# Kernel tuning notes

Measured on AMD Instinct MI355X. Metric: run time of the kernel, lower is better.

Reference implementation:

```python
import jax, jax.numpy as jnp
import numpy as np

N = 256      # Lx * Ly sites
NH = 64      # GRU hidden units
K = 2        # local Hilbert space dim


def setup_inputs() -> dict:
    key = jax.random.key(0)
    k1, k2, k3, k4, k5 = jax.random.split(key, 5)
    # scale weights down to keep sigmoid/tanh/softmax in a sane range
    return {
        "numsamples": 8192,
        "Wi": jax.random.normal(k1, (K, 3 * NH), jnp.float32) * 0.1,
        "Wh": jax.random.normal(k2, (NH, 3 * NH), jnp.float32) * 0.1,
        "b": jax.random.normal(k3, (2, 3 * NH), jnp.float32) * 0.1,
        "Wd": jax.random.normal(k4, (NH, K), jnp.float32) * 0.1,
        "bd": jax.random.normal(k5, (K,), jnp.float32) * 0.1,
    }


def _gru_cell(x, h, Wi, Wh, b):
    # keras GRU with reset_after=True (default)
    mx = x @ Wi + b[0]           # [B, 3*NH]
    mh = h @ Wh + b[1]           # [B, 3*NH]
    xz, xr, xh = jnp.split(mx, 3, axis=-1)
    rz, rr, rh = jnp.split(mh, 3, axis=-1)
    z = jax.nn.sigmoid(xz + rz)
    r = jax.nn.sigmoid(xr + rr)
    hh = jnp.tanh(xh + r * rh)
    return z * h + (1.0 - z) * hh


def reference(numsamples, Wi, Wh, b, Wd, bd):
    B = numsamples
    keys = jax.random.split(jax.random.key(1234), N)

    def step(carry, key):
        h, inp = carry                         # h: [B,NH], inp: [B,K] one-hot
        h = _gru_cell(inp, h, Wi, Wh, b)
        logits = h @ Wd + bd                   # [B,K]
        logp = jax.nn.log_softmax(logits)      # log of dense-softmax output
        s = jax.random.categorical(key, logits)  # [B] int
        chosen = jnp.take_along_axis(logp, s[:, None], axis=1)[:, 0]
        inp_new = jax.nn.one_hot(s, K, dtype=jnp.float32)
        return (h, inp_new), (s, chosen)

    h0 = jnp.zeros((B, NH), jnp.float32)
    inp0 = jnp.zeros((B, K), jnp.float32)
    _, (samples, chosen_logp) = jax.lax.scan(step, (h0, inp0), keys)
    samples = samples.T.astype(jnp.float32)           # [B, N]
    log_probs = 0.5 * jnp.sum(chosen_logp, axis=0)    # [B]
    return samples, log_probs
```

## Files before the change

kernel.cpp:

```cpp
#include <hip/hip_runtime.h>
#include <stdint.h>

#define NSITES 256
#define NHID   64
#define BATCH  8192

typedef float v4f __attribute__((ext_vector_type(4)));
typedef short v8s __attribute__((ext_vector_type(8)));

__device__ __forceinline__ uint32_t rotl32(uint32_t v, int d) {
  return (v << d) | (v >> (32 - d));
}

__device__ __forceinline__ void tf2x32(uint32_t k0, uint32_t k1,
                                       uint32_t x0, uint32_t x1,
                                       uint32_t& o0, uint32_t& o1) {
  uint32_t ks2 = k0 ^ k1 ^ 0x1BD11BDAu;
  x0 += k0; x1 += k1;
#define TFR4(a,b,c,d) \
  x0 += x1; x1 = rotl32(x1,a); x1 ^= x0; \
  x0 += x1; x1 = rotl32(x1,b); x1 ^= x0; \
  x0 += x1; x1 = rotl32(x1,c); x1 ^= x0; \
  x0 += x1; x1 = rotl32(x1,d); x1 ^= x0;
  TFR4(13,15,26,6)   x0 += k1;  x1 += ks2 + 1u;
  TFR4(17,29,16,24)  x0 += ks2; x1 += k0  + 2u;
  TFR4(13,15,26,6)   x0 += k0;  x1 += k1  + 3u;
  TFR4(17,29,16,24)  x0 += k1;  x1 += ks2 + 4u;
  TFR4(13,15,26,6)   x0 += ks2; x1 += k0  + 5u;
#undef TFR4
  o0 = x0; o1 = x1;
}

__device__ __forceinline__ float gumb_from_bits(uint32_t bits) {
  float f = __uint_as_float((bits >> 9) | 0x3f800000u) - 1.0f;
  float u = (f == 0.0f) ? 1.17549435e-38f : f;
  return -logf(-logf(u));
}

__device__ __forceinline__ uint32_t rbits32(uint32_t k0, uint32_t k1, uint32_t e) {
  uint32_t a, b;
  tf2x32(k0, k1, 0u, e, a, b);
  return a ^ b;
}

__global__ void split_awt(const float* __restrict__ Wh, const float* __restrict__ Wd,
                          ushort* __restrict__ w0, ushort* __restrict__ w1,
                          ushort* __restrict__ w2) {
  int idx = blockIdx.x * 256 + threadIdx.x;
  if (idx >= 208 * 64) return;
  int col = idx >> 6;
  int j   = idx & 63;
  float w;
  if (col < 192) {
    w = Wh[j * 192 + col];
  } else {
    const int which = (col - 192) & 3;
    w = (which == 0) ? Wd[j * 2] : (which == 1) ? Wd[j * 2 + 1] : 0.0f;
  }
  uint32_t u0 = __float_as_uint(w) & 0xffff0000u;
  float f0 = __uint_as_float(u0);
  float r1 = w - f0;
  uint32_t u1 = __float_as_uint(r1) & 0xffff0000u;
  float f1 = __uint_as_float(u1);
  float r2 = r1 - f1;
  uint32_t u2 = __float_as_uint(r2) & 0xffff0000u;
  w0[idx] = (ushort)(u0 >> 16);
  w1[idx] = (ushort)(u1 >> 16);
  w2[idx] = (ushort)(u2 >> 16);
}

__device__ __forceinline__ float sigmoid_xla(float x) {
  return 0.5f + 0.5f * tanhf(0.5f * x);
}

#define MF(A_, B_, C_) __builtin_amdgcn_mfma_f32_16x16x32_bf16((A_), (B_), (C_), 0, 0, 0)
#define F4(v_, r_) (((const float*)&(v_))[r_])

__global__ __launch_bounds__(256, 2)
void rnn_mfma9(const float* __restrict__ Wi, const float* __restrict__ bb,
               const float* __restrict__ bd,
               const ushort* __restrict__ w0p, const ushort* __restrict__ w1p,
               const ushort* __restrict__ w2p,
               float* __restrict__ out_s, float* __restrict__ out_lp) {
  __shared__ __align__(16) ushort bsp[2][3072];
  __shared__ __align__(16) float2 gl[NSITES * 16];
  __shared__ __align__(16) float c0zr[128];
  __shared__ __align__(16) float bh0a[64], bh1a[64];
  __shared__ __align__(16) float cw0[192], cw1[192];

  const int tid = threadIdx.x;
  const int l = tid & 63, s = l & 15, hi = l >> 4;
  const int w = tid >> 6;
  const int base = blockIdx.x * 16;

  if (tid < 64) {
    c0zr[tid] = bb[tid] + bb[192 + tid];
    c0zr[tid + 64] = bb[tid + 64] + bb[256 + tid];
    bh0a[tid] = bb[128 + tid];
    bh1a[tid] = bb[320 + tid];
    cw0[tid] = Wi[tid]; cw0[tid + 64] = Wi[tid + 64]; cw0[tid + 128] = Wi[tid + 128];
    cw1[tid] = Wi[192 + tid]; cw1[tid + 64] = Wi[256 + tid]; cw1[tid + 128] = Wi[320 + tid];
  }
  for (int k = tid; k < 1536; k += 256) ((uint*)bsp[0])[k] = 0u;

  {
    uint32_t kt0, kt1;
    tf2x32(0u, 1234u, 0u, (uint32_t)tid, kt0, kt1);
    for (int k = 0; k < 16; ++k) {
      const int bidx = base + k;
      const float g0 = gumb_from_bits(rbits32(kt0, kt1, (uint32_t)(2 * bidx)));
      const float g1 = gumb_from_bits(rbits32(kt0, kt1, (uint32_t)(2 * bidx + 1)));
      gl[tid * 16 + k] = make_float2(g0, g1);
    }
  }
  __syncthreads();

  v8s A0[3][2], A1[3][2], A2[3][2];
#pragma unroll
  for (int i3 = 0; i3 < 3; ++i3) {
    const int tile = w + 4 * i3;
#pragma unroll
    for (int kc = 0; kc < 2; ++kc) {
      const int off = (16 * tile + s) * 64 + 32 * kc + 8 * hi;
      A0[i3][kc] = *reinterpret_cast<const v8s*>(w0p + off);
      A1[i3][kc] = *reinterpret_cast<const v8s*>(w1p + off);
      A2[i3][kc] = *reinterpret_cast<const v8s*>(w2p + off);
    }
  }
  v8s L0[2], L1[2], L2[2];
#pragma unroll
  for (int kc = 0; kc < 2; ++kc) {
    const int off = (192 + s) * 64 + 32 * kc + 8 * hi;
    L0[kc] = *reinterpret_cast<const v8s*>(w0p + off);
    L1[kc] = *reinterpret_cast<const v8s*>(w1p + off);
    L2[kc] = *reinterpret_cast<const v8s*>(w2p + off);
  }

  const float bd0 = bd[0], bd1 = bd[1];
  const int u0i = 16 * w + 4 * hi;
  const float4 czv  = *reinterpret_cast<const float4*>(&c0zr[u0i]);
  const float4 crv  = *reinterpret_cast<const float4*>(&c0zr[64 + u0i]);
  const float4 bh0v = *reinterpret_cast<const float4*>(&bh0a[u0i]);
  const float4 bh1v = *reinterpret_cast<const float4*>(&bh1a[u0i]);
  const float4 wz0  = *reinterpret_cast<const float4*>(&cw0[u0i]);
  const float4 wz1  = *reinterpret_cast<const float4*>(&cw1[u0i]);
  const float4 wr0  = *reinterpret_cast<const float4*>(&cw0[64 + u0i]);
  const float4 wr1  = *reinterpret_cast<const float4*>(&cw1[64 + u0i]);
  const float4 wh0  = *reinterpret_cast<const float4*>(&cw0[128 + u0i]);
  const float4 wh1  = *reinterpret_cast<const float4*>(&cw1[128 + u0i]);

  const int kcw = w >> 1;
  const int hgw = (2 * w + (hi >> 1)) & 3;
  const int i0  = (hi & 1) * 4;

  float hreg[4] = {0.0f, 0.0f, 0.0f, 0.0f};
  float lp = 0.0f;
  int p = 0;

  for (int t = 0; t <= NSITES; ++t) {
    const ushort* rb = bsp[p] + hi * 128 + s * 8;
    v8s B0[2], B1[2], B2[2];
#pragma unroll
    for (int kc = 0; kc < 2; ++kc) {
      B0[kc] = *reinterpret_cast<const v8s*>(rb + kc * 512);
      B1[kc] = *reinterpret_cast<const v8s*>(rb + 1024 + kc * 512);
      B2[kc] = *reinterpret_cast<const v8s*>(rb + 2048 + kc * 512);
    }

    v4f al = {0.0f, 0.0f, 0.0f, 0.0f};
#pragma unroll
    for (int kc = 0; kc < 2; ++kc) al = MF(L1[kc], B1[kc], al);
#pragma unroll
    for (int kc = 0; kc < 2; ++kc) al = MF(L2[kc], B0[kc], al);
#pragma unroll
    for (int kc = 0; kc < 2; ++kc) al = MF(L0[kc], B2[kc], al);
#pragma unroll
    for (int kc = 0; kc < 2; ++kc) al = MF(L1[kc], B0[kc], al);
#pragma unroll
    for (int kc = 0; kc < 2; ++kc) al = MF(L0[kc], B1[kc], al);
#pragma unroll
    for (int kc = 0; kc < 2; ++kc) al = MF(L0[kc], B0[kc], al);

    v4f acc[3];
    if (t < NSITES) {
#pragma unroll
      for (int i3 = 0; i3 < 3; ++i3) {
        v4f a = {0.0f, 0.0f, 0.0f, 0.0f};
#pragma unroll
        for (int kc = 0; kc < 2; ++kc) a = MF(A2[i3][kc], B0[kc], a);
#pragma unroll
        for (int kc = 0; kc < 2; ++kc) a = MF(A0[i3][kc], B2[kc], a);
#pragma unroll
        for (int kc = 0; kc < 2; ++kc) a = MF(A1[i3][kc], B1[kc], a);
#pragma unroll
        for (int kc = 0; kc < 2; ++kc) a = MF(A1[i3][kc], B0[kc], a);
#pragma unroll
        for (int kc = 0; kc < 2; ++kc) a = MF(A0[i3][kc], B1[kc], a);
#pragma unroll
        for (int kc = 0; kc < 2; ++kc) a = MF(A0[i3][kc], B0[kc], a);
        acc[i3] = a;
      }
    }

    int scd = 0;
    if (t > 0) {
      const float2 gc = gl[(t - 1) * 16 + s];
      const float l0 = al[0] + bd0, l1 = al[1] + bd1;
      const float mmax = fmaxf(l0, l1);
      const float sh0 = l0 - mmax, sh1 = l1 - mmax;
      const float lse = logf(expf(sh0) + expf(sh1));
      scd = ((l1 + gc.y) > (l0 + gc.x)) ? 1 : 0;
      lp += (scd ? sh1 : sh0) - lse;
      if (tid < 16) out_s[(size_t)(base + s) * NSITES + (t - 1)] = (float)scd;
    }

    if (t < NSITES) {
      float selz[4], selr[4], selh[4];
      if (t == 0) {
#pragma unroll
        for (int r = 0; r < 4; ++r) { selz[r] = 0.0f; selr[r] = 0.0f; selh[r] = 0.0f; }
      } else {
#pragma unroll
        for (int r = 0; r < 4; ++r) {
          selz[r] = scd ? F4(wz1, r) : F4(wz0, r);
          selr[r] = scd ? F4(wr1, r) : F4(wr0, r);
          selh[r] = scd ? F4(wh1, r) : F4(wh0, r);
        }
      }

      uint sp0[4], sp1[4], sp2[4];
#pragma unroll
      for (int r = 0; r < 4; ++r) {
        const float zin = acc[0][r] + F4(czv, r) + selz[r];
        const float rin = acc[1][r] + F4(crv, r) + selr[r];
        const float rhv = acc[2][r] + F4(bh1v, r);
        const float xhv = F4(bh0v, r) + selh[r];
        const float zg = sigmoid_xla(zin);
        const float rg = sigmoid_xla(rin);
        const float hg = tanhf(xhv + rg * rhv);
        const float hn = zg * hreg[r] + (1.0f - zg) * hg;
        hreg[r] = hn;
        const uint u0 = __float_as_uint(hn) & 0xffff0000u;
        const float f0 = __uint_as_float(u0);
        const float r1f = hn - f0;
        const uint u1 = __float_as_uint(r1f) & 0xffff0000u;
        const float f1 = __uint_as_float(u1);
        const float r2f = r1f - f1;
        const uint u2 = __float_as_uint(r2f) & 0xffff0000u;
        sp0[r] = u0 >> 16; sp1[r] = u1 >> 16; sp2[r] = u2 >> 16;
      }
      ushort* wb = bsp[p ^ 1] + kcw * 512 + hgw * 128 + s * 8 + i0;
      {
        uint2 q;
        q.x = sp0[0] | (sp0[1] << 16); q.y = sp0[2] | (sp0[3] << 16);
        *reinterpret_cast<uint2*>(wb) = q;
        q.x = sp1[0] | (sp1[1] << 16); q.y = sp1[2] | (sp1[3] << 16);
        *reinterpret_cast<uint2*>(wb + 1024) = q;
        q.x = sp2[0] | (sp2[1] << 16); q.y = sp2[2] | (sp2[3] << 16);
        *reinterpret_cast<uint2*>(wb + 2048) = q;
      }
    }

    __syncthreads();
    p ^= 1;
  }

  if (tid < 16) out_lp[base + s] = 0.5f * lp;
}

__global__ __launch_bounds__(64)
void rnn_plain(const float* __restrict__ Wi, const float* __restrict__ Wh,
               const float* __restrict__ bb, const float* __restrict__ Wd,
               const float* __restrict__ bd,
               float* __restrict__ out_s, float* __restrict__ out_lp) {
  const int lane = threadIdx.x;
  const int b = blockIdx.x;

  float wz[NHID], wr[NHID], wh[NHID];
#pragma unroll
  for (int j = 0; j < NHID; ++j) {
    wz[j] = Wh[j * 192 + lane];
    wr[j] = Wh[j * 192 + 64 + lane];
    wh[j] = Wh[j * 192 + 128 + lane];
  }
  const float b1z = bb[192 + lane];
  const float b1r = bb[192 + 64 + lane];
  const float b1h = bb[192 + 128 + lane];
  const float m0z = bb[lane], m0r = bb[64 + lane], m0h = bb[128 + lane];
  const float m1z = Wi[lane] + m0z, m1r = Wi[64 + lane] + m0r, m1h = Wi[128 + lane] + m0h;
  const float m2z = Wi[192 + lane] + m0z, m2r = Wi[192 + 64 + lane] + m0r,
              m2h = Wi[192 + 128 + lane] + m0h;
  const float wd0 = Wd[lane * 2 + 0], wd1 = Wd[lane * 2 + 1];
  const float bd0 = bd[0], bd1 = bd[1];

  float h = 0.0f, lpsum = 0.0f;
  float xz = m0z, xr = m0r, xh = m0h;

  for (int t = 0; t < NSITES; ++t) {
    uint32_t kt0, kt1;
    tf2x32(0u, 1234u, 0u, (uint32_t)t, kt0, kt1);
    const float g0 = gumb_from_bits(rbits32(kt0, kt1, (uint32_t)(2 * b)));
    const float g1 = gumb_from_bits(rbits32(kt0, kt1, (uint32_t)(2 * b + 1)));

    float az = 0.0f, ar = 0.0f, ah = 0.0f;
#pragma unroll
    for (int j = 0; j < NHID; ++j) {
      const float hj = __int_as_float(__builtin_amdgcn_readlane(__float_as_int(h), j));
      az = fmaf(hj, wz[j], az);
      ar = fmaf(hj, wr[j], ar);
      ah = fmaf(hj, wh[j], ah);
    }
    const float rz = az + b1z, rr = ar + b1r, rh = ah + b1h;
    const float zg = sigmoid_xla(xz + rz);
    const float rg = sigmoid_xla(xr + rr);
    const float hg = tanhf(xh + rg * rh);
    h = zg * h + (1.0f - zg) * hg;

    float p0 = h * wd0, p1 = h * wd1;
#pragma unroll
    for (int off = 32; off > 0; off >>= 1) {
      p0 += __shfl_xor(p0, off, 64);
      p1 += __shfl_xor(p1, off, 64);
    }
    const float l0 = p0 + bd0, l1 = p1 + bd1;
    const float mmax = fmaxf(l0, l1);
    const float sh0 = l0 - mmax, sh1 = l1 - mmax;
    const float lse = logf(expf(sh0) + expf(sh1));
    const int si = ((l1 + g1) > (l0 + g0)) ? 1 : 0;
    lpsum += (si ? sh1 : sh0) - lse;
    if (lane == 0) out_s[(size_t)b * NSITES + t] = (float)si;
    xz = si ? m2z : m1z;
    xr = si ? m2r : m1r;
    xh = si ? m2h : m1h;
  }

  if (lane == 0) out_lp[b] = 0.5f * lpsum;
}

extern "C" void kernel_launch(void* const* d_in, const int* in_sizes, int n_in,
                              void* d_out, int out_size, void* d_ws, size_t ws_size,
                              hipStream_t stream) {
  const float* Wi = (const float*)d_in[1];
  const float* Wh = (const float*)d_in[2];
  const float* bb = (const float*)d_in[3];
  const float* Wd = (const float*)d_in[4];
  const float* bd = (const float*)d_in[5];

  float* out    = (float*)d_out;
  float* out_s  = out;
  float* out_lp = out + (size_t)BATCH * NSITES;

  const size_t wb = (size_t)208 * 64 * sizeof(ushort);

  if (ws_size >= 3 * wb) {
    ushort* w0 = (ushort*)d_ws;
    ushort* w1 = w0 + 208 * 64;
    ushort* w2 = w1 + 208 * 64;
    split_awt<<<(208 * 64 + 255) / 256, 256, 0, stream>>>(Wh, Wd, w0, w1, w2);
    rnn_mfma9<<<BATCH / 16, 256, 0, stream>>>(Wi, bb, bd, w0, w1, w2, out_s, out_lp);
  } else {
    rnn_plain<<<BATCH, 64, 0, stream>>>(Wi, Wh, bb, Wd, bd, out_s, out_lp);
  }
}
```

Baseline: 402.9 us.

## Process two interleaved 16-sample groups per block to hide serial latency

```diff
diff --git a/kernel.cpp b/kernel.cpp
--- a/kernel.cpp
+++ b/kernel.cpp
@@ -73,17 +73,31 @@
   return 0.5f + 0.5f * tanhf(0.5f * x);
 }
 
+__device__ __forceinline__ void gen_gl(float2* gl, int base, int tid, int phase) {
+  const int st = phase * 128 + (tid & 127);
+  const int kb = (tid >> 7) * 16;
+  uint32_t kt0, kt1;
+  tf2x32(0u, 1234u, 0u, (uint32_t)st, kt0, kt1);
+  for (int k = 0; k < 16; ++k) {
+    const int bidx = base + kb + k;
+    const float g0 = gumb_from_bits(rbits32(kt0, kt1, (uint32_t)(2 * bidx)));
+    const float g1 = gumb_from_bits(rbits32(kt0, kt1, (uint32_t)(2 * bidx + 1)));
+    gl[(tid & 127) * 32 + kb + k] = make_float2(g0, g1);
+  }
+}
+
 #define MF(A_, B_, C_) __builtin_amdgcn_mfma_f32_16x16x32_bf16((A_), (B_), (C_), 0, 0, 0)
 #define F4(v_, r_) (((const float*)&(v_))[r_])
 
 __global__ __launch_bounds__(256, 2)
-void rnn_mfma9(const float* __restrict__ Wi, const float* __restrict__ bb,
-               const float* __restrict__ bd,
-               const ushort* __restrict__ w0p, const ushort* __restrict__ w1p,
-               const ushort* __restrict__ w2p,
-               float* __restrict__ out_s, float* __restrict__ out_lp) {
-  __shared__ __align__(16) ushort bsp[2][3072];
-  __shared__ __align__(16) float2 gl[NSITES * 16];
+void rnn_mfma11(const float* __restrict__ Wi, const float* __restrict__ bb,
+                const float* __restrict__ bd,
+                const ushort* __restrict__ w0p, const ushort* __restrict__ w1p,
+                const ushort* __restrict__ w2p,
+                float* __restrict__ out_s, float* __restrict__ out_lp) {
+  __shared__ __align__(16) ushort bspX[2][3072];
+  __shared__ __align__(16) ushort bspY[2][3072];
+  __shared__ __align__(16) float2 gl[128 * 32];
   __shared__ __align__(16) float c0zr[128];
   __shared__ __align__(16) float bh0a[64], bh1a[64];
   __shared__ __align__(16) float cw0[192], cw1[192];
@@ -91,7 +105,7 @@
   const int tid = threadIdx.x;
   const int l = tid & 63, s = l & 15, hi = l >> 4;
   const int w = tid >> 6;
-  const int base = blockIdx.x * 16;
+  const int base = blockIdx.x * 32;
 
   if (tid < 64) {
     c0zr[tid] = bb[tid] + bb[192 + tid];
@@ -101,18 +115,11 @@
     cw0[tid] = Wi[tid]; cw0[tid + 64] = Wi[tid + 64]; cw0[tid + 128] = Wi[tid + 128];
     cw1[tid] = Wi[192 + tid]; cw1[tid + 64] = Wi[256 + tid]; cw1[tid + 128] = Wi[320 + tid];
   }
-  for (int k = tid; k < 1536; k += 256) ((uint*)bsp[0])[k] = 0u;
-
-  {
-    uint32_t kt0, kt1;
-    tf2x32(0u, 1234u, 0u, (uint32_t)tid, kt0, kt1);
-    for (int k = 0; k < 16; ++k) {
-      const int bidx = base + k;
-      const float g0 = gumb_from_bits(rbits32(kt0, kt1, (uint32_t)(2 * bidx)));
-      const float g1 = gumb_from_bits(rbits32(kt0, kt1, (uint32_t)(2 * bidx + 1)));
-      gl[tid * 16 + k] = make_float2(g0, g1);
-    }
-  }
+  for (int k = tid; k < 1536; k += 256) {
+    ((uint*)bspX[0])[k] = 0u;
+    ((uint*)bspY[0])[k] = 0u;
+  }
+  gen_gl(gl, base, tid, 0);
   __syncthreads();
 
   v8s A0[3][2], A1[3][2], A2[3][2];
@@ -153,104 +160,154 @@
   const int hgw = (2 * w + (hi >> 1)) & 3;
   const int i0  = (hi & 1) * 4;
 
-  float hreg[4] = {0.0f, 0.0f, 0.0f, 0.0f};
-  float lp = 0.0f;
+  float hregX[4] = {0.0f, 0.0f, 0.0f, 0.0f};
+  float hregY[4] = {0.0f, 0.0f, 0.0f, 0.0f};
+  float lpX = 0.0f, lpY = 0.0f;
   int p = 0;
 
   for (int t = 0; t <= NSITES; ++t) {
-    const ushort* rb = bsp[p] + hi * 128 + s * 8;
-    v8s B0[2], B1[2], B2[2];
+    float2 gcX = make_float2(0.0f, 0.0f), gcY = make_float2(0.0f, 0.0f);
+    if (t > 0) {
+      const int gsl = ((t - 1) & 127) * 32;
+      gcX = gl[gsl + s];
+      gcY = gl[gsl + 16 + s];
+    }
+    if (t == 128) {
+      __syncthreads();
+      gen_gl(gl, base, tid, 1);
+    }
+
+    const ushort* rbX = bspX[p] + hi * 128 + s * 8;
+    v8s B0X[2], B1X[2], B2X[2];
 #pragma unroll
     for (int kc = 0; kc < 2; ++kc) {
-      B0[kc] = *reinterpret_cast<const v8s*>(rb + kc * 512);
-      B1[kc] = *reinterpret_cast<const v8s*>(rb + 1024 + kc * 512);
-      B2[kc] = *reinterpret_cast<const v8s*>(rb + 2048 + kc * 512);
-    }
-
-    v4f al = {0.0f, 0.0f, 0.0f, 0.0f};
-#pragma unroll
-    for (int kc = 0; kc < 2; ++kc) al = MF(L1[kc], B1[kc], al);
-#pragma unroll
-    for (int kc = 0; kc < 2; ++kc) al = MF(L2[kc], B0[kc], al);
-#pragma unroll
-    for (int kc = 0; kc < 2; ++kc) al = MF(L0[kc], B2[kc], al);
-#pragma unroll
-    for (int kc = 0; kc < 2; ++kc) al = MF(L1[kc], B0[kc], al);
-#pragma unroll
-    for (int kc = 0; kc < 2; ++kc) al = MF(L0[kc], B1[kc], al);
-#pragma unroll
-    for (int kc = 0; kc < 2; ++kc) al = MF(L0[kc], B0[kc], al);
-
-    v4f acc[3];
+      B0X[kc] = *reinterpret_cast<const v8s*>(rbX + kc * 512);
+      B1X[kc] = *reinterpret_cast<const v8s*>(rbX + 1024 + kc * 512);
+      B2X[kc] = *reinterpret_cast<const v8s*>(rbX + 2048 + kc * 512);
+    }
+    v4f alX = {0.0f, 0.0f, 0.0f, 0.0f};
+#pragma unroll
+    for (int kc = 0; kc < 2; ++kc) alX = MF(L1[kc], B1X[kc], alX);
+#pragma unroll
+    for (int kc = 0; kc < 2; ++kc) alX = MF(L2[kc], B0X[kc], alX);
+#pragma unroll
+    for (int kc = 0; kc < 2; ++kc) alX = MF(L0[kc], B2X[kc], alX);
+#pragma unroll
+    for (int kc = 0; kc < 2; ++kc) alX = MF(L1[kc], B0X[kc], alX);
+#pragma unroll
+    for (int kc = 0; kc < 2; ++kc) alX = MF(L0[kc], B1X[kc], alX);
+#pragma unroll
+    for (int kc = 0; kc < 2; ++kc) alX = MF(L0[kc], B0X[kc], alX);
+
+    v4f accX[3];
     if (t < NSITES) {
 #pragma unroll
       for (int i3 = 0; i3 < 3; ++i3) {
         v4f a = {0.0f, 0.0f, 0.0f, 0.0f};
 #pragma unroll
-        for (int kc = 0; kc < 2; ++kc) a = MF(A2[i3][kc], B0[kc], a);
-#pragma unroll
-        for (int kc = 0; kc < 2; ++kc) a = MF(A0[i3][kc], B2[kc], a);
-#pragma unroll
-        for (int kc = 0; kc < 2; ++kc) a = MF(A1[i3][kc], B1[kc], a);
-#pragma unroll
-        for (int kc = 0; kc < 2; ++kc) a = MF(A1[i3][kc], B0[kc], a);
-#pragma unroll
-        for (int kc = 0; kc < 2; ++kc) a = MF(A0[i3][kc], B1[kc], a);
-#pragma unroll
-        for (int kc = 0; kc < 2; ++kc) a = MF(A0[i3][kc], B0[kc], a);
-        acc[i3] = a;
+        for (int kc = 0; kc < 2; ++kc) a = MF(A2[i3][kc], B0X[kc], a);
+#pragma unroll
+        for (int kc = 0; kc < 2; ++kc) a = MF(A0[i3][kc], B2X[kc], a);
+#pragma unroll
+        for (int kc = 0; kc < 2; ++kc) a = MF(A1[i3][kc], B1X[kc], a);
+#pragma unroll
+        for (int kc = 0; kc < 2; ++kc) a = MF(A1[i3][kc], B0X[kc], a);
+#pragma unroll
+        for (int kc = 0; kc < 2; ++kc) a = MF(A0[i3][kc], B1X[kc], a);
+#pragma unroll
+        for (int kc = 0; kc < 2; ++kc) a = MF(A0[i3][kc], B0X[kc], a);
+        accX[i3] = a;
       }
     }
 
-    int scd = 0;
+    const ushort* rbY = bspY[p] + hi * 128 + s * 8;
+    v8s B0Y[2], B1Y[2], B2Y[2];
+#pragma unroll
+    for (int kc = 0; kc < 2; ++kc) {
+      B0Y[kc] = *reinterpret_cast<const v8s*>(rbY + kc * 512);
+      B1Y[kc] = *reinterpret_cast<const v8s*>(rbY + 1024 + kc * 512);
+      B2Y[kc] = *reinterpret_cast<const v8s*>(rbY + 2048 + kc * 512);
+    }
+    v4f alY = {0.0f, 0.0f, 0.0f, 0.0f};
+#pragma unroll
+    for (int kc = 0; kc < 2; ++kc) alY = MF(L1[kc], B1Y[kc], alY);
+#pragma unroll
+    for (int kc = 0; kc < 2; ++kc) alY = MF(L2[kc], B0Y[kc], alY);
+#pragma unroll
+    for (int kc = 0; kc < 2; ++kc) alY = MF(L0[kc], B2Y[kc], alY);
+#pragma unroll
+    for (int kc = 0; kc < 2; ++kc) alY = MF(L1[kc], B0Y[kc], alY);
+#pragma unroll
+    for (int kc = 0; kc < 2; ++kc) alY = MF(L0[kc], B1Y[kc], alY);
+#pragma unroll
+    for (int kc = 0; kc < 2; ++kc) alY = MF(L0[kc], B0Y[kc], alY);
+
+    v4f accY[3];
+    if (t < NSITES) {
+#pragma unroll
+      for (int i3 = 0; i3 < 3; ++i3) {
+        v4f a = {0.0f, 0.0f, 0.0f, 0.0f};
+#pragma unroll
+        for (int kc = 0; kc < 2; ++kc) a = MF(A2[i3][kc], B0Y[kc], a);
+#pragma unroll
+        for (int kc = 0; kc < 2; ++kc) a = MF(A0[i3][kc], B2Y[kc], a);
+#pragma unroll
+        for (int kc = 0; kc < 2; ++kc) a = MF(A1[i3][kc], B1Y[kc], a);
+#pragma unroll
+        for (int kc = 0; kc < 2; ++kc) a = MF(A1[i3][kc], B0Y[kc], a);
+#pragma unroll
+        for (int kc = 0; kc < 2; ++kc) a = MF(A0[i3][kc], B1Y[kc], a);
+#pragma unroll
+        for (int kc = 0; kc < 2; ++kc) a = MF(A0[i3][kc], B0Y[kc], a);
+        accY[i3] = a;
+      }
+    }
+
+    int scdX = 0, scdY = 0;
+    float l0X = 0.0f, l1X = 0.0f, l0Y = 0.0f, l1Y = 0.0f;
     if (t > 0) {
-      const float2 gc = gl[(t - 1) * 16 + s];
-      const float l0 = al[0] + bd0, l1 = al[1] + bd1;
-      const float mmax = fmaxf(l0, l1);
-      const float sh0 = l0 - mmax, sh1 = l1 - mmax;
-      const float lse = logf(expf(sh0) + expf(sh1));
-      scd = ((l1 + gc.y) > (l0 + gc.x)) ? 1 : 0;
-      lp += (scd ? sh1 : sh0) - lse;
-      if (tid < 16) out_s[(size_t)(base + s) * NSITES + (t - 1)] = (float)scd;
+      l0X = alX[0] + bd0; l1X = alX[1] + bd1;
+      scdX = ((l1X + gcX.y) > (l0X + gcX.x)) ? 1 : 0;
+      l0Y = alY[0] + bd0; l1Y = alY[1] + bd1;
+      scdY = ((l1Y + gcY.y) > (l0Y + gcY.x)) ? 1 : 0;
     }
 
     if (t < NSITES) {
-      float selz[4], selr[4], selh[4];
-      if (t == 0) {
-#pragma unroll
-        for (int r = 0; r < 4; ++r) { selz[r] = 0.0f; selr[r] = 0.0f; selh[r] = 0.0f; }
-      } else {
+      {
+        float selz[4], selr[4], selh[4];
+        if (t == 0) {
+#pragma unroll
+          for (int r = 0; r < 4; ++r) { selz[r] = 0.0f; selr[r] = 0.0f; selh[r] = 0.0f; }
+        } else {
+#pragma unroll
+          for (int r = 0; r < 4; ++r) {
+            selz[r] = scdX ? F4(wz1, r) : F4(wz0, r);
+            selr[r] = scdX ? F4(wr1, r) : F4(wr0, r);
+            selh[r] = scdX ? F4(wh1, r) : F4(wh0, r);
+          }
+        }
+        uint sp0[4], sp1[4], sp2[4];
 #pragma unroll
         for (int r = 0; r < 4; ++r) {
-          selz[r] = scd ? F4(wz1, r) : F4(wz0, r);
-          selr[r] = scd ? F4(wr1, r) : F4(wr0, r);
-          selh[r] = scd ? F4(wh1, r) : F4(wh0, r);
+          const float zin = accX[0][r] + F4(czv, r) + selz[r];
+          const float rin = accX[1][r] + F4(crv, r) + selr[r];
+          const float rhv = accX[2][r] + F4(bh1v, r);
+          const float xhv = F4(bh0v, r) + selh[r];
+          const float zg = sigmoid_xla(zin);
+          const float rg = sigmoid_xla(rin);
+          const float hg = tanhf(xhv + rg * rhv);
+          const float hn = zg * hregX[r] + (1.0f - zg) * hg;
+          hregX[r] = hn;
+          const uint u0 = __float_as_uint(hn) & 0xffff0000u;
+          const float f0 = __uint_as_float(u0);
+          const float r1f = hn - f0;
+          const uint u1 = __float_as_uint(r1f) & 0xffff0000u;
+          const float f1 = __uint_as_float(u1);
+          const float r2f = r1f - f1;
+          const uint u2 = __float_as_uint(r2f) & 0xffff0000u;
+          sp0[r] = u0 >> 16; sp1[r] = u1 >> 16; sp2[r] = u2 >> 16;
         }
-      }
-
-      uint sp0[4], sp1[4], sp2[4];
-#pragma unroll
-      for (int r = 0; r < 4; ++r) {
-        const float zin = acc[0][r] + F4(czv, r) + selz[r];
-        const float rin = acc[1][r] + F4(crv, r) + selr[r];
-        const float rhv = acc[2][r] + F4(bh1v, r);
-        const float xhv = F4(bh0v, r) + selh[r];
-        const float zg = sigmoid_xla(zin);
-        const float rg = sigmoid_xla(rin);
-        const float hg = tanhf(xhv + rg * rhv);
-        const float hn = zg * hreg[r] + (1.0f - zg) * hg;
-        hreg[r] = hn;
-        const uint u0 = __float_as_uint(hn) & 0xffff0000u;
-        const float f0 = __uint_as_float(u0);
-        const float r1f = hn - f0;
-        const uint u1 = __float_as_uint(r1f) & 0xffff0000u;
-        const float f1 = __uint_as_float(u1);
-        const float r2f = r1f - f1;
-        const uint u2 = __float_as_uint(r2f) & 0xffff0000u;
-        sp0[r] = u0 >> 16; sp1[r] = u1 >> 16; sp2[r] = u2 >> 16;
-      }
-      ushort* wb = bsp[p ^ 1] + kcw * 512 + hgw * 128 + s * 8 + i0;
-      {
+        ushort* wb = bspX[p ^ 1] + kcw * 512 + hgw * 128 + s * 8 + i0;
         uint2 q;
         q.x = sp0[0] | (sp0[1] << 16); q.y = sp0[2] | (sp0[3] << 16);
         *reinterpret_cast<uint2*>(wb) = q;
@@ -259,13 +316,74 @@
         q.x = sp2[0] | (sp2[1] << 16); q.y = sp2[2] | (sp2[3] << 16);
         *reinterpret_cast<uint2*>(wb + 2048) = q;
       }
+      {
+        float selz[4], selr[4], selh[4];
+        if (t == 0) {
+#pragma unroll
+          for (int r = 0; r < 4; ++r) { selz[r] = 0.0f; selr[r] = 0.0f; selh[r] = 0.0f; }
+        } else {
+#pragma unroll
+          for (int r = 0; r < 4; ++r) {
+            selz[r] = scdY ? F4(wz1, r) : F4(wz0, r);
+            selr[r] = scdY ? F4(wr1, r) : F4(wr0, r);
+            selh[r] = scdY ? F4(wh1, r) : F4(wh0, r);
+          }
+        }
+        uint sp0[4], sp1[4], sp2[4];
+#pragma unroll
+        for (int r = 0; r < 4; ++r) {
+          const float zin = accY[0][r] + F4(czv, r) + selz[r];
+          const float rin = accY[1][r] + F4(crv, r) + selr[r];
+          const float rhv = accY[2][r] + F4(bh1v, r);
+          const float xhv = F4(bh0v, r) + selh[r];
+          const float zg = sigmoid_xla(zin);
+          const float rg = sigmoid_xla(rin);
+          const float hg = tanhf(xhv + rg * rhv);
+          const float hn = zg * hregY[r] + (1.0f - zg) * hg;
+          hregY[r] = hn;
+          const uint u0 = __float_as_uint(hn) & 0xffff0000u;
+          const float f0 = __uint_as_float(u0);
+          const float r1f = hn - f0;
+          const uint u1 = __float_as_uint(r1f) & 0xffff0000u;
+          const float f1 = __uint_as_float(u1);
+          const float r2f = r1f - f1;
+          const uint u2 = __float_as_uint(r2f) & 0xffff0000u;
+          sp0[r] = u0 >> 16; sp1[r] = u1 >> 16; sp2[r] = u2 >> 16;
+        }
+        ushort* wb = bspY[p ^ 1] + kcw * 512 + hgw * 128 + s * 8 + i0;
+        uint2 q;
+        q.x = sp0[0] | (sp0[1] << 16); q.y = sp0[2] | (sp0[3] << 16);
+        *reinterpret_cast<uint2*>(wb) = q;
+        q.x = sp1[0] | (sp1[1] << 16); q.y = sp1[2] | (sp1[3] << 16);
+        *reinterpret_cast<uint2*>(wb + 1024) = q;
+        q.x = sp2[0] | (sp2[1] << 16); q.y = sp2[2] | (sp2[3] << 16);
+        *reinterpret_cast<uint2*>(wb + 2048) = q;
+      }
+    }
+
+    if (t > 0) {
+      const float mmX = fmaxf(l0X, l1X);
+      const float sh0X = l0X - mmX, sh1X = l1X - mmX;
+      const float lseX = logf(expf(sh0X) + expf(sh1X));
+      lpX += (scdX ? sh1X : sh0X) - lseX;
+      const float mmY = fmaxf(l0Y, l1Y);
+      const float sh0Y = l0Y - mmY, sh1Y = l1Y - mmY;
+      const float lseY = logf(expf(sh0Y) + expf(sh1Y));
+      lpY += (scdY ? sh1Y : sh0Y) - lseY;
+      if (tid < 16) {
+        out_s[(size_t)(base + s) * NSITES + (t - 1)] = (float)scdX;
+        out_s[(size_t)(base + 16 + s) * NSITES + (t - 1)] = (float)scdY;
+      }
     }
 
     __syncthreads();
     p ^= 1;
   }
 
-  if (tid < 16) out_lp[base + s] = 0.5f * lp;
+  if (tid < 16) {
+    out_lp[base + s] = 0.5f * lpX;
+    out_lp[base + 16 + s] = 0.5f * lpY;
+  }
 }
 
 __global__ __launch_bounds__(64)
@@ -357,7 +475,7 @@
     ushort* w1 = w0 + 208 * 64;
     ushort* w2 = w1 + 208 * 64;
     split_awt<<<(208 * 64 + 255) / 256, 256, 0, stream>>>(Wh, Wd, w0, w1, w2);
-    rnn_mfma9<<<BATCH / 16, 256, 0, stream>>>(Wi, bb, bd, w0, w1, w2, out_s, out_lp);
+    rnn_mfma11<<<BATCH / 32, 256, 0, stream>>>(Wi, bb, bd, w0, w1, w2, out_s, out_lp);
   } else {
     rnn_plain<<<BATCH, 64, 0, stream>>>(Wi, Wh, bb, Wd, bd, out_s, out_lp);
   }
```

New measurement: 659.2 us. +63.6%, slower.
